# Kernel tuning notes

Measured on AMD Instinct MI355X. Metric: run time of the kernel, lower is better.

## Reference

```python
import jax, jax.numpy as jnp
import numpy as np

D_MODEL = 512
N_HEADS = 8
D_K = D_MODEL // N_HEADS  # 64
EPS = 1e-5


def setup_inputs() -> dict:
    key = jax.random.key(0)
    ks = jax.random.split(key, 16)
    s = 0.02
    B, T = 4, 2048
    return {
        "x": jax.random.normal(ks[0], (B, T, D_MODEL), dtype=jnp.float32),
        # per-head q/k/v projections stacked over heads: [H, d_model, d_k]
        "Wq": jax.random.normal(ks[1], (N_HEADS, D_MODEL, D_K), dtype=jnp.float32) * s,
        "bq": jnp.zeros((N_HEADS, D_K), dtype=jnp.float32),
        "Wk": jax.random.normal(ks[2], (N_HEADS, D_MODEL, D_K), dtype=jnp.float32) * s,
        "bk": jnp.zeros((N_HEADS, D_K), dtype=jnp.float32),
        "Wv": jax.random.normal(ks[3], (N_HEADS, D_MODEL, D_K), dtype=jnp.float32) * s,
        "bv": jnp.zeros((N_HEADS, D_K), dtype=jnp.float32),
        "Wp": jax.random.normal(ks[4], (D_MODEL, D_MODEL), dtype=jnp.float32) * s,
        "bp": jnp.zeros((D_MODEL,), dtype=jnp.float32),
        "W1": jax.random.normal(ks[5], (D_MODEL, 4 * D_MODEL), dtype=jnp.float32) * s,
        "b1": jnp.zeros((4 * D_MODEL,), dtype=jnp.float32),
        "W2": jax.random.normal(ks[6], (4 * D_MODEL, D_MODEL), dtype=jnp.float32) * s,
        "b2": jnp.zeros((D_MODEL,), dtype=jnp.float32),
        "g1": jnp.ones((D_MODEL,), dtype=jnp.float32),
        "be1": jnp.zeros((D_MODEL,), dtype=jnp.float32),
        "g2": jnp.ones((D_MODEL,), dtype=jnp.float32),
        "be2": jnp.zeros((D_MODEL,), dtype=jnp.float32),
    }


def _layer_norm(x, g, b):
    mu = jnp.mean(x, axis=-1, keepdims=True)
    var = jnp.var(x, axis=-1, keepdims=True)
    return (x - mu) * jax.lax.rsqrt(var + EPS) * g + b


def _block(x, Wq, bq, Wk, bk, Wv, bv, Wp, bp, W1, b1, W2, b2, g1, be1, g2, be2):
    B, T, _ = x.shape
    h = _layer_norm(x, g1, be1)
    # batched per-head projections: [B, H, T, d_k]
    q = jnp.einsum('btd,hdk->bhtk', h, Wq) + bq[:, None, :]
    k = jnp.einsum('btd,hdk->bhtk', h, Wk) + bk[:, None, :]
    v = jnp.einsum('btd,hdk->bhtk', h, Wv) + bv[:, None, :]
    scores = jnp.einsum('bhtk,bhsk->bhts', q, k)  # [B, H, T, T]
    causal = jnp.tril(jnp.ones((T, T), dtype=bool))
    # faithful to source: mask with -1e9 BEFORE dividing by sqrt(d_k)
    scores = jnp.where(causal, scores, jnp.float32(-1e9))
    attn = jax.nn.softmax(scores / jnp.float32(np.sqrt(D_K)), axis=-1)
    o = jnp.einsum('bhts,bhsk->bhtk', attn, v)  # [B, H, T, d_k]
    o = o.transpose(0, 2, 1, 3).reshape(B, T, D_MODEL)  # concat heads
    x = x + o @ Wp + bp
    h2 = _layer_norm(x, g2, be2)
    ff = jax.nn.relu(h2 @ W1 + b1) @ W2 + b2
    return x + ff


def reference(x, Wq, bq, Wk, bk, Wv, bv, Wp, bp, W1, b1, W2, b2, g1, be1, g2, be2):
    return _block(x, Wq, bq, Wk, bk, Wv, bv, Wp, bp, W1, b1, W2, b2, g1, be1, g2, be2)
```

## Files before the change

### kernel.cpp

```cpp
#include <hip/hip_runtime.h>
#include <hip/hip_bf16.h>
#include <math.h>

#define BATCH 4
#define SEQ   2048
#define DM    512
#define NH    8
#define DK    64
#define FF    2048
#define BT    (BATCH * SEQ)

#define SCALE_Q 0.18033688011112042f

typedef short bf16x8 __attribute__((ext_vector_type(8)));
typedef float f32x4  __attribute__((ext_vector_type(4)));

static __device__ inline short f2bf(float f) {
  union { float f; unsigned u; } v; v.f = f;
  unsigned r = (v.u + 0x7fffu + ((v.u >> 16) & 1u)) >> 16;
  return (short)r;
}

static __device__ __forceinline__ void gload16(const short* g, short* l) {
  __builtin_amdgcn_global_load_lds(
      (const __attribute__((address_space(1))) void*)g,
      (__attribute__((address_space(3))) void*)l, 16, 0, 0);
}

static __device__ __forceinline__ void xcd_swizzle(int& bx, int& by) {
  int gx = gridDim.x;
  int nwg = gx * gridDim.y;
  int id = blockIdx.x + gx * blockIdx.y;
  int nid = (id & 7) * (nwg >> 3) + (id >> 3);
  bx = nid % gx;
  by = nid / gx;
}

__global__ __launch_bounds__(256) void ln_kernel(
    const float* __restrict__ x, const float* __restrict__ gamma,
    const float* __restrict__ beta, short* __restrict__ out) {
  int row = blockIdx.x;
  const float* xr = x + (size_t)row * DM;
  int t = threadIdx.x;
  float v0 = xr[t], v1 = xr[t + 256];
  float s = v0 + v1;
  float sq = v0 * v0 + v1 * v1;
  for (int off = 32; off; off >>= 1) {
    s  += __shfl_xor(s, off);
    sq += __shfl_xor(sq, off);
  }
  __shared__ float ssum[4], ssq[4];
  int wave = t >> 6, lane = t & 63;
  if (lane == 0) { ssum[wave] = s; ssq[wave] = sq; }
  __syncthreads();
  if (t == 0) {
    float S = ssum[0] + ssum[1] + ssum[2] + ssum[3];
    float Q = ssq[0] + ssq[1] + ssq[2] + ssq[3];
    float mu = S * (1.0f / DM);
    float var = Q * (1.0f / DM) - mu * mu;
    ssum[0] = mu;
    ssq[0] = rsqrtf(var + 1e-5f);
  }
  __syncthreads();
  float mu = ssum[0], rstd = ssq[0];
  short* orow = out + (size_t)row * DM;
  orow[t]       = f2bf((v0 - mu) * rstd * gamma[t]       + beta[t]);
  orow[t + 256] = f2bf((v1 - mu) * rstd * gamma[t + 256] + beta[t + 256]);
}

__global__ __launch_bounds__(256) void wconv_kernel(
    const float* Wq, const float* Wk, const float* Wv,
    const float* Wp, const float* W1, const float* W2,
    short* wqkv, short* wpt, short* w1t, short* w2t) {
  int id = blockIdx.x;
  const float* src; short* dst; int R, C, tx, ty;
  if (id < 192) {
    int z = id >> 3;
    int m = z >> 3, hh = z & 7;
    const float* s0 = (m == 0) ? Wq : (m == 1) ? Wk : Wv;
    src = s0 + (size_t)hh * 512 * 64;
    dst = wqkv + ((size_t)(m * 512 + hh * 64)) * 512;
    R = 512; C = 64; tx = 0; ty = id & 7;
  } else if (id < 256) {
    int w = id - 192; src = Wp; dst = wpt; R = 512; C = 512;
    tx = w & 7; ty = w >> 3;
  } else if (id < 512) {
    int w = id - 256; src = W1; dst = w1t; R = 512; C = 2048;
    tx = w & 31; ty = w >> 5;
  } else {
    int w = id - 512; src = W2; dst = w2t; R = 2048; C = 512;
    tx = w & 7; ty = w >> 3;
  }
  __shared__ float Ts[64][68];
  int t = threadIdx.x;
  int r = t >> 2, c0 = (t & 3) * 16;
  const float* sp = src + (size_t)(ty * 64 + r) * C + tx * 64 + c0;
#pragma unroll
  for (int i = 0; i < 16; i += 4) {
    float4 v = *(const float4*)(sp + i);
    Ts[c0 + i + 0][r] = v.x; Ts[c0 + i + 1][r] = v.y;
    Ts[c0 + i + 2][r] = v.z; Ts[c0 + i + 3][r] = v.w;
  }
  __syncthreads();
  short* dp = dst + (size_t)(tx * 64 + r) * R + ty * 64 + c0;
  short tmp[16];
#pragma unroll
  for (int i = 0; i < 16; ++i) tmp[i] = f2bf(Ts[r][c0 + i]);
  *(int4*)(dp)     = *(int4*)&tmp[0];
  *(int4*)(dp + 8) = *(int4*)&tmp[8];
}

template<int TM, int TN>
__device__ __forceinline__ void gemm_core(
    const short* __restrict__ A, const short* __restrict__ Bw,
    int m0, int n0, int K, short* smem, f32x4 (&acc)[TM / 32][TN / 32]) {
  constexpr int AF = TM / 32, BF = TN / 32;
  constexpr int AC = TM / 64, BC = TN / 64;
  constexpr int BUFS = (TM + TN) * 32;
  int t = threadIdx.x;
  int wave = t >> 6, lane = t & 63, quad = lane >> 4, l16 = lane & 15;
  int wr = wave >> 1, wc = wave & 1;

  size_t aoff[AC], boff[BC];
  int aldsoff[AC], bldsoff[BC];
#pragma unroll
  for (int c = 0; c < AC; ++c) {
    int p = c * 256 + t, row = p >> 2, lg = (p & 3) ^ ((row >> 1) & 3);
    aoff[c] = (size_t)(m0 + row) * K + lg * 8;
    aldsoff[c] = c * 2048 + wave * 512;
  }
#pragma unroll
  for (int c = 0; c < BC; ++c) {
    int p = c * 256 + t, row = p >> 2, lg = (p & 3) ^ ((row >> 1) & 3);
    boff[c] = (size_t)(n0 + row) * K + lg * 8;
    bldsoff[c] = TM * 32 + c * 2048 + wave * 512;
  }

#pragma unroll
  for (int c = 0; c < AC; ++c) gload16(A + aoff[c], smem + aldsoff[c]);
#pragma unroll
  for (int c = 0; c < BC; ++c) gload16(Bw + boff[c], smem + bldsoff[c]);

  int physo = (quad ^ ((l16 >> 1) & 3)) * 8;

  for (int k0 = 0; k0 < K; k0 += 32) {
    short* cbuf = smem + ((k0 >> 5) & 1) * BUFS;
    __syncthreads();
    if (k0 + 32 < K) {
      short* nbuf = smem + (((k0 >> 5) & 1) ^ 1) * BUFS;
#pragma unroll
      for (int c = 0; c < AC; ++c) gload16(A + aoff[c] + k0 + 32, nbuf + aldsoff[c]);
#pragma unroll
      for (int c = 0; c < BC; ++c) gload16(Bw + boff[c] + k0 + 32, nbuf + bldsoff[c]);
    }
    bf16x8 af[AF], bfr[BF];
#pragma unroll
    for (int i = 0; i < AF; ++i)
      af[i] = *(const bf16x8*)&cbuf[(wr * (TM / 2) + i * 16 + l16) * 32 + physo];
#pragma unroll
    for (int j = 0; j < BF; ++j)
      bfr[j] = *(const bf16x8*)&cbuf[TM * 32 + (wc * (TN / 2) + j * 16 + l16) * 32 + physo];
#pragma unroll
    for (int i = 0; i < AF; ++i)
#pragma unroll
      for (int j = 0; j < BF; ++j)
        acc[i][j] = __builtin_amdgcn_mfma_f32_16x16x32_bf16(bfr[j], af[i], acc[i][j], 0, 0, 0);
  }
}

__global__ __launch_bounds__(256) void mgemm64_kernel(
    const short* __restrict__ A, const short* __restrict__ Bw,
    const float* __restrict__ bias, const float* __restrict__ res,
    void* __restrict__ C, int N, int K, int dorelu, int bf16out) {
  __shared__ __align__(16) short smem[2 * 8192];
  f32x4 acc[2][2];
  f32x4 zf = {0.f, 0.f, 0.f, 0.f};
#pragma unroll
  for (int i = 0; i < 2; ++i)
#pragma unroll
    for (int j = 0; j < 2; ++j) acc[i][j] = zf;
  int bx, by;
  xcd_swizzle(bx, by);
  int m0 = by * 64, n0 = bx * 64;

  int t = threadIdx.x;
  int wave = t >> 6, lane = t & 63, quad = lane >> 4, l16 = lane & 15;
  int wr = wave >> 1, wc = wave & 1;

  int rA0 = t >> 3,        lg0 = (t & 7) ^ (rA0 & 7);
  int rA1 = 32 + (t >> 3), lg1 = (t & 7) ^ (rA1 & 7);
  size_t aoff0 = (size_t)(m0 + rA0) * K + lg0 * 8;
  size_t aoff1 = (size_t)(m0 + rA1) * K + lg1 * 8;
  size_t boff0 = (size_t)(n0 + rA0) * K + lg0 * 8;
  size_t boff1 = (size_t)(n0 + rA1) * K + lg1 * 8;
  int lo0 = wave * 512, lo1 = 2048 + wave * 512;

  gload16(A + aoff0, smem + lo0);
  gload16(A + aoff1, smem + lo1);
  gload16(Bw + boff0, smem + 4096 + lo0);
  gload16(Bw + boff1, smem + 4096 + lo1);

  int sw = l16 & 7;

  for (int k0 = 0; k0 < K; k0 += 64) {
    short* cbuf = smem + ((k0 >> 6) & 1) * 8192;
    __syncthreads();
    if (k0 + 64 < K) {
      short* nbuf = smem + (((k0 >> 6) & 1) ^ 1) * 8192;
      gload16(A + aoff0 + k0 + 64, nbuf + lo0);
      gload16(A + aoff1 + k0 + 64, nbuf + lo1);
      gload16(Bw + boff0 + k0 + 64, nbuf + 4096 + lo0);
      gload16(Bw + boff1 + k0 + 64, nbuf + 4096 + lo1);
    }
    bf16x8 af0[2], af1[2], bf0[2], bf1[2];
#pragma unroll
    for (int i = 0; i < 2; ++i) {
      int r = wr * 32 + i * 16 + l16;
      af0[i] = *(const bf16x8*)&cbuf[r * 64 + ((quad ^ sw) * 8)];
      af1[i] = *(const bf16x8*)&cbuf[r * 64 + (((4 + quad) ^ sw) * 8)];
    }
#pragma unroll
    for (int j = 0; j < 2; ++j) {
      int r = wc * 32 + j * 16 + l16;
      bf0[j] = *(const bf16x8*)&cbuf[4096 + r * 64 + ((quad ^ sw) * 8)];
      bf1[j] = *(const bf16x8*)&cbuf[4096 + r * 64 + (((4 + quad) ^ sw) * 8)];
    }
#pragma unroll
    for (int i = 0; i < 2; ++i)
#pragma unroll
      for (int j = 0; j < 2; ++j) {
        acc[i][j] = __builtin_amdgcn_mfma_f32_16x16x32_bf16(bf0[j], af0[i], acc[i][j], 0, 0, 0);
        acc[i][j] = __builtin_amdgcn_mfma_f32_16x16x32_bf16(bf1[j], af1[i], acc[i][j], 0, 0, 0);
      }
  }

#pragma unroll
  for (int i = 0; i < 2; ++i) {
    int m = m0 + wr * 32 + i * 16 + l16;
#pragma unroll
    for (int j = 0; j < 2; ++j) {
      int nb = n0 + wc * 32 + j * 16 + quad * 4;
      float4 bv = *(const float4*)&bias[nb];
      float v[4] = {acc[i][j][0] + bv.x, acc[i][j][1] + bv.y,
                    acc[i][j][2] + bv.z, acc[i][j][3] + bv.w};
      if (dorelu) {
#pragma unroll
        for (int r = 0; r < 4; ++r) v[r] = fmaxf(v[r], 0.0f);
      }
      size_t off = (size_t)m * N + nb;
      if (res) {
        float4 rv = *(const float4*)(res + off);
        v[0] += rv.x; v[1] += rv.y; v[2] += rv.z; v[3] += rv.w;
      }
      if (bf16out) {
        short tmp[4] = {f2bf(v[0]), f2bf(v[1]), f2bf(v[2]), f2bf(v[3])};
        *(int2*)((short*)C + off) = *(int2*)tmp;
      } else {
        float4 outv = {v[0], v[1], v[2], v[3]};
        *(float4*)((float*)C + off) = outv;
      }
    }
  }
}

__global__ __launch_bounds__(256) void qkv_kernel(
    const short* __restrict__ A, const short* __restrict__ Bw,
    const float* __restrict__ bq, const float* __restrict__ bk,
    const float* __restrict__ bv,
    short* __restrict__ q, short* __restrict__ k, short* __restrict__ vt) {
  __shared__ __align__(16) short smem[12288];
  f32x4 acc[4][2];
  f32x4 zf = {0.f, 0.f, 0.f, 0.f};
#pragma unroll
  for (int i = 0; i < 4; ++i)
#pragma unroll
    for (int j = 0; j < 2; ++j) acc[i][j] = zf;
  int bx, by;
  xcd_swizzle(bx, by);
  int m0 = by * 128, n0 = bx * 64;
  gemm_core<128, 64>(A, Bw, m0, n0, DM, smem, acc);

  int t = threadIdx.x;
  int wave = t >> 6, lane = t & 63, quad = lane >> 4, l16 = lane & 15;
  int wr = wave >> 1, wc = wave & 1;

  if (n0 < 1024) {
    short* out = (n0 < 512) ? q : k;
    const float* bias = (n0 < 512) ? bq + n0 : bk + (n0 - 512);
    float scale = (n0 < 512) ? SCALE_Q : 1.0f;
    int ncol0 = (n0 < 512) ? n0 : n0 - 512;
#pragma unroll
    for (int i = 0; i < 4; ++i) {
      int m = m0 + wr * 64 + i * 16 + l16;
#pragma unroll
      for (int j = 0; j < 2; ++j) {
        int nb = wc * 32 + j * 16 + quad * 4;
        float4 bvv = *(const float4*)&bias[nb];
        short tmp[4];
        tmp[0] = f2bf((acc[i][j][0] + bvv.x) * scale);
        tmp[1] = f2bf((acc[i][j][1] + bvv.y) * scale);
        tmp[2] = f2bf((acc[i][j][2] + bvv.z) * scale);
        tmp[3] = f2bf((acc[i][j][3] + bvv.w) * scale);
        *(int2*)(out + (size_t)m * DM + ncol0 + nb) = *(int2*)tmp;
      }
    }
  } else {
    const float* bias = bv + (n0 - 1024);
    __syncthreads();
    short* Ts = smem;
#pragma unroll
    for (int i = 0; i < 4; ++i) {
      int ml = wr * 64 + i * 16 + l16;
#pragma unroll
      for (int j = 0; j < 2; ++j) {
        int nb = wc * 32 + j * 16 + quad * 4;
        float4 bvv = *(const float4*)&bias[nb];
        Ts[(nb + 0) * 136 + ml] = f2bf(acc[i][j][0] + bvv.x);
        Ts[(nb + 1) * 136 + ml] = f2bf(acc[i][j][1] + bvv.y);
        Ts[(nb + 2) * 136 + ml] = f2bf(acc[i][j][2] + bvv.z);
        Ts[(nb + 3) * 136 + ml] = f2bf(acc[i][j][3] + bvv.w);
      }
    }
    __syncthreads();
    int nl = t >> 2, seg = (t & 3) * 32;
    int gn = (n0 - 1024) + nl;
    int hh = gn >> 6, dk = gn & 63;
    int bidx = m0 >> 11, s0 = (m0 & 2047) + seg;
    short* dst = vt + ((size_t)((bidx * NH + hh) * DK + dk)) * SEQ + s0;
    const short* srcT = &Ts[nl * 136 + seg];
#pragma unroll
    for (int i2 = 0; i2 < 32; i2 += 8)
      *(int4*)(dst + i2) = *(const int4*)(srcT + i2);
  }
}

template<bool DIAG>
static __device__ __forceinline__ void attn_tile(
    const short* __restrict__ KsC, const short* __restrict__ VsC,
    short* __restrict__ Psw, const bf16x8& qf0, const bf16x8& qf1,
    f32x4 (&o_acc)[4], float& l_part, int quad, int l16,
    int keyb0, int qrow) {
  f32x4 zf = {0.f, 0.f, 0.f, 0.f};
  int sw = l16 & 7;

#pragma unroll
  for (int nt = 0; nt < 4; ++nt) {
    int krow = nt * 16 + l16;
    bf16x8 ka0 = *(const bf16x8*)&KsC[krow * 64 + ((quad ^ sw) * 8)];
    bf16x8 ka1 = *(const bf16x8*)&KsC[krow * 64 + (((4 + quad) ^ sw) * 8)];
    f32x4 s = __builtin_amdgcn_mfma_f32_16x16x32_bf16(ka0, qf0, zf, 0, 0, 0);
    s = __builtin_amdgcn_mfma_f32_16x16x32_bf16(ka1, qf1, s, 0, 0, 0);
    int keyb = keyb0 + nt * 16 + quad * 4;
    float pr[4];
#pragma unroll
    for (int r = 0; r < 4; ++r) {
      float e = exp2f(s[r]);
      pr[r] = (DIAG && (keyb + r > qrow)) ? 0.0f : e;
      l_part += pr[r];
    }
    unsigned pk0 = __builtin_amdgcn_perm(
        __float_as_uint(pr[1]), __float_as_uint(pr[0]), 0x07060302u);
    unsigned pk1 = __builtin_amdgcn_perm(
        __float_as_uint(pr[3]), __float_as_uint(pr[2]), 0x07060302u);
    int2 w = {(int)pk0, (int)pk1};
    *(int2*)&Psw[l16 * 64 + (((nt * 2 + (quad >> 1)) ^ sw) << 3) +
                 ((quad & 1) * 4)] = w;
  }

  bf16x8 apf0 = *(const bf16x8*)&Psw[l16 * 64 + ((quad ^ sw) * 8)];
  bf16x8 apf1 = *(const bf16x8*)&Psw[l16 * 64 + (((4 + quad) ^ sw) * 8)];
  __builtin_amdgcn_s_setprio(1);
#pragma unroll
  for (int nt2 = 0; nt2 < 4; ++nt2) {
    int vrow = nt2 * 16 + l16;
    bf16x8 vf0 = *(const bf16x8*)&VsC[vrow * 64 + ((quad ^ sw) * 8)];
    bf16x8 vf1 = *(const bf16x8*)&VsC[vrow * 64 + (((4 + quad) ^ sw) * 8)];
    o_acc[nt2] = __builtin_amdgcn_mfma_f32_16x16x32_bf16(vf0, apf0, o_acc[nt2], 0, 0, 0);
    o_acc[nt2] = __builtin_amdgcn_mfma_f32_16x16x32_bf16(vf1, apf1, o_acc[nt2], 0, 0, 0);
  }
  __builtin_amdgcn_s_setprio(0);
}

__global__ __launch_bounds__(256) void fattn_kernel(
    const short* __restrict__ Q, const short* __restrict__ Kg,
    const short* __restrict__ Vt, short* __restrict__ O) {
  int id = blockIdx.x + 32 * (blockIdx.y + NH * blockIdx.z);
  int c = id & 7, j = id >> 3;
  int g = c * 4 + (j & 3);
  int qt = 31 - (j >> 2);
  int h = g & 7, b = g >> 3;
  int q0 = qt * 64;
  int t = threadIdx.x, wave = t >> 6, lane = t & 63, quad = lane >> 4, l16 = lane & 15;

  __shared__ __align__(16) short Ks[2][64 * 64];
  __shared__ __align__(16) short Vs[2][64 * 64];
  __shared__ __align__(16) short Ps[4][16 * 64];

  f32x4 zf = {0.f, 0.f, 0.f, 0.f};
  const short* qp = Q + ((size_t)(b * SEQ + q0 + wave * 16 + l16)) * DM + h * DK;
  bf16x8 qf0 = *(const bf16x8*)(qp + quad * 8);
  bf16x8 qf1 = *(const bf16x8*)(qp + 32 + quad * 8);

  f32x4 o_acc[4];
  float l_part = 0.0f;
#pragma unroll
  for (int i = 0; i < 4; ++i) o_acc[i] = zf;

  const short* kb = Kg + ((size_t)(b * SEQ)) * DM + h * DK;
  const short* vb = Vt + ((size_t)((b * NH + h) * DK)) * SEQ;

  int row0 = t >> 3,         lg0 = (t & 7) ^ (row0 & 7);
  int row1 = (256 + t) >> 3, lg1 = ((256 + t) & 7) ^ (row1 & 7);
  const short* kp0 = kb + (size_t)row0 * DM + lg0 * 8;
  const short* kp1 = kb + (size_t)row1 * DM + lg1 * 8;
  const short* vp0 = vb + (size_t)row0 * SEQ + lg0 * 8;
  const short* vp1 = vb + (size_t)row1 * SEQ + lg1 * 8;
  int lo0 = wave * 512, lo1 = 2048 + wave * 512;

#define STAGE_KV(B) do {                                     \
    gload16(kp0, &Ks[B][lo0]); gload16(kp1, &Ks[B][lo1]);    \
    gload16(vp0, &Vs[B][lo0]); gload16(vp1, &Vs[B][lo1]);    \
    kp0 += 64 * DM; kp1 += 64 * DM; vp0 += 64; vp1 += 64; } while (0)

  STAGE_KV(0);

  int qrow = q0 + wave * 16 + l16;
  short* Psw = &Ps[wave][0];

  int buf = 0;
  for (int kt = 0; kt < qt; ++kt) {
    __syncthreads();
    STAGE_KV(buf ^ 1);
    attn_tile<false>(&Ks[buf][0], &Vs[buf][0], Psw, qf0, qf1,
                     o_acc, l_part, quad, l16, 0, qrow);
    buf ^= 1;
  }
  __syncthreads();
  attn_tile<true>(&Ks[buf][0], &Vs[buf][0], Psw, qf0, qf1,
                  o_acc, l_part, quad, l16, qt * 64, qrow);

  float lf = l_part;
  lf += __shfl_xor(lf, 16);
  lf += __shfl_xor(lf, 32);
  float inv = 1.0f / lf;
  short* orow = O + ((size_t)(b * SEQ) + qrow) * DM + h * DK;
#pragma unroll
  for (int nt2 = 0; nt2 < 4; ++nt2) {
    short tmp[4];
#pragma unroll
    for (int r = 0; r < 4; ++r) tmp[r] = f2bf(o_acc[nt2][r] * inv);
    *(int2*)(orow + nt2 * 16 + quad * 4) = *(int2*)tmp;
  }
#undef STAGE_KV
}

extern "C" void kernel_launch(void* const* d_in, const int* in_sizes, int n_in,
                              void* d_out, int out_size, void* d_ws, size_t ws_size,
                              hipStream_t stream) {
  const float* x   = (const float*)d_in[0];
  const float* Wq  = (const float*)d_in[1];
  const float* bq  = (const float*)d_in[2];
  const float* Wk  = (const float*)d_in[3];
  const float* bk  = (const float*)d_in[4];
  const float* Wv  = (const float*)d_in[5];
  const float* bv  = (const float*)d_in[6];
  const float* Wp  = (const float*)d_in[7];
  const float* bp  = (const float*)d_in[8];
  const float* W1  = (const float*)d_in[9];
  const float* b1  = (const float*)d_in[10];
  const float* W2  = (const float*)d_in[11];
  const float* b2  = (const float*)d_in[12];
  const float* g1  = (const float*)d_in[13];
  const float* be1 = (const float*)d_in[14];
  const float* g2  = (const float*)d_in[15];
  const float* be2 = (const float*)d_in[16];
  float* out = (float*)d_out;

  char* wsb = (char*)d_ws;
  const size_t SB = (size_t)BT * DM * 2;
  short* h    = (short*)(wsb);
  short* q    = (short*)(wsb + SB);
  short* k    = (short*)(wsb + 2 * SB);
  short* vt   = (short*)(wsb + 3 * SB);
  short* o    = (short*)(wsb + 4 * SB);
  float* x2   = (float*)(wsb + 5 * SB);
  short* h2   = (short*)(wsb + 5 * SB + (size_t)BT * DM * 4);
  short* ff   = (short*)(wsb + 6 * SB + (size_t)BT * DM * 4);
  short* wqkv = (short*)(wsb + 6 * SB + (size_t)BT * DM * 4 + (size_t)BT * FF * 2);
  short* wpt  = wqkv + 1536 * 512;
  short* w1t  = wpt + 512 * 512;
  short* w2t  = w1t + 2048 * 512;

  dim3 blk(256);

  wconv_kernel<<<dim3(768), blk, 0, stream>>>(Wq, Wk, Wv, Wp, W1, W2,
                                              wqkv, wpt, w1t, w2t);
  ln_kernel<<<BT, blk, 0, stream>>>(x, g1, be1, h);

  qkv_kernel<<<dim3(24, 64), blk, 0, stream>>>(h, wqkv, bq, bk, bv, q, k, vt);

  fattn_kernel<<<dim3(32, NH, BATCH), blk, 0, stream>>>(q, k, vt, o);

  mgemm64_kernel<<<dim3(8, 128), blk, 0, stream>>>(o, wpt, bp, x, x2, DM, DM, 0, 0);
  ln_kernel<<<BT, blk, 0, stream>>>(x2, g2, be2, h2);
  mgemm64_kernel<<<dim3(32, 128), blk, 0, stream>>>(h2, w1t, b1, nullptr, ff, FF, DM, 1, 1);
  mgemm64_kernel<<<dim3(8, 128), blk, 0, stream>>>(ff, w2t, b2, x2, out, DM, FF, 0, 0);
}
```

Baseline: 254.5 us.

## Split long causal attention query tiles across two blocks with a combine pass

Query tiles 16-31 are split into two key ranges (tiles 0-15 and 16-diagonal) handled by separate blocks. Each half writes unnormalized fp32 partial outputs and row sums to scratch that reuses the FF buffer, and a new combine kernel sums them and normalizes. The aim is to even out per-block work in causal attention and raise the block count from 1024 to 1536, cutting the tail where a few long blocks run alone. The cost is an extra kernel launch and extra fp32 scratch traffic. Adding the two partials directly is only valid because the kernel uses no per-row running max rescaling.

```diff
diff --git a/kernel.cpp b/kernel.cpp
--- a/kernel.cpp
+++ b/kernel.cpp
@@ -383,12 +383,19 @@
 
 __global__ __launch_bounds__(256) void fattn_kernel(
     const short* __restrict__ Q, const short* __restrict__ Kg,
-    const short* __restrict__ Vt, short* __restrict__ O) {
-  int id = blockIdx.x + 32 * (blockIdx.y + NH * blockIdx.z);
+    const short* __restrict__ Vt, short* __restrict__ O,
+    float* __restrict__ pscr) {
+  int id = blockIdx.x;
   int c = id & 7, j = id >> 3;
-  int g = c * 4 + (j & 3);
-  int qt = 31 - (j >> 2);
+  int sub = j & 3, w = j >> 2;
+  int g = c * 4 + sub;
   int h = g & 7, b = g >> 3;
+  int qt, kt0, ktN, p = 0;
+  bool split;
+  if (w < 16)      { qt = 31 - w;        p = 0; kt0 = 0;  ktN = 16;     split = true;  }
+  else if (w < 32) { qt = 31 - (w - 16); p = 1; kt0 = 16; ktN = qt + 1; split = true;  }
+  else             { qt = 15 - (w - 32);        kt0 = 0;  ktN = qt + 1; split = false; }
+  bool hasdiag = !(split && p == 0);
   int q0 = qt * 64;
   int t = threadIdx.x, wave = t >> 6, lane = t & 63, quad = lane >> 4, l16 = lane & 15;
 
@@ -411,10 +418,10 @@
 
   int row0 = t >> 3,         lg0 = (t & 7) ^ (row0 & 7);
   int row1 = (256 + t) >> 3, lg1 = ((256 + t) & 7) ^ (row1 & 7);
-  const short* kp0 = kb + (size_t)row0 * DM + lg0 * 8;
-  const short* kp1 = kb + (size_t)row1 * DM + lg1 * 8;
-  const short* vp0 = vb + (size_t)row0 * SEQ + lg0 * 8;
-  const short* vp1 = vb + (size_t)row1 * SEQ + lg1 * 8;
+  const short* kp0 = kb + (size_t)row0 * DM + lg0 * 8 + (size_t)kt0 * 64 * DM;
+  const short* kp1 = kb + (size_t)row1 * DM + lg1 * 8 + (size_t)kt0 * 64 * DM;
+  const short* vp0 = vb + (size_t)row0 * SEQ + lg0 * 8 + kt0 * 64;
+  const short* vp1 = vb + (size_t)row1 * SEQ + lg1 * 8 + kt0 * 64;
   int lo0 = wave * 512, lo1 = 2048 + wave * 512;
 
 #define STAGE_KV(B) do {                                     \
@@ -428,7 +435,7 @@
   short* Psw = &Ps[wave][0];
 
   int buf = 0;
-  for (int kt = 0; kt < qt; ++kt) {
+  for (int kt = kt0; kt < ktN - 1; ++kt) {
     __syncthreads();
     STAGE_KV(buf ^ 1);
     attn_tile<false>(&Ks[buf][0], &Vs[buf][0], Psw, qf0, qf1,
@@ -436,22 +443,55 @@
     buf ^= 1;
   }
   __syncthreads();
-  attn_tile<true>(&Ks[buf][0], &Vs[buf][0], Psw, qf0, qf1,
-                  o_acc, l_part, quad, l16, qt * 64, qrow);
+  if (hasdiag)
+    attn_tile<true>(&Ks[buf][0], &Vs[buf][0], Psw, qf0, qf1,
+                    o_acc, l_part, quad, l16, (ktN - 1) * 64, qrow);
+  else
+    attn_tile<false>(&Ks[buf][0], &Vs[buf][0], Psw, qf0, qf1,
+                     o_acc, l_part, quad, l16, 0, qrow);
 
   float lf = l_part;
   lf += __shfl_xor(lf, 16);
   lf += __shfl_xor(lf, 32);
-  float inv = 1.0f / lf;
-  short* orow = O + ((size_t)(b * SEQ) + qrow) * DM + h * DK;
-#pragma unroll
-  for (int nt2 = 0; nt2 < 4; ++nt2) {
-    short tmp[4];
-#pragma unroll
-    for (int r = 0; r < 4; ++r) tmp[r] = f2bf(o_acc[nt2][r] * inv);
-    *(int2*)(orow + nt2 * 16 + quad * 4) = *(int2*)tmp;
+
+  if (!split) {
+    float inv = 1.0f / lf;
+    short* orow = O + ((size_t)(b * SEQ) + qrow) * DM + h * DK;
+#pragma unroll
+    for (int nt2 = 0; nt2 < 4; ++nt2) {
+      short tmp[4];
+#pragma unroll
+      for (int r = 0; r < 4; ++r) tmp[r] = f2bf(o_acc[nt2][r] * inv);
+      *(int2*)(orow + nt2 * 16 + quad * 4) = *(int2*)tmp;
+    }
+  } else {
+    int pblk = g * 16 + (qt - 16);
+    int srow = pblk * 64 + wave * 16 + l16;
+    float* po = pscr + (size_t)p * (32768 * 64);
+    float* pl = pscr + (size_t)2 * (32768 * 64) + (size_t)p * 32768;
+#pragma unroll
+    for (int nt2 = 0; nt2 < 4; ++nt2)
+      *(f32x4*)&po[(size_t)srow * 64 + nt2 * 16 + quad * 4] = o_acc[nt2];
+    if (lane < 16) pl[pblk * 64 + wave * 16 + lane] = lf;
   }
 #undef STAGE_KV
+}
+
+__global__ __launch_bounds__(256) void cmb_kernel(
+    const float* __restrict__ pscr, short* __restrict__ O) {
+  int gid = blockIdx.x * 256 + threadIdx.x;
+  int srow = gid >> 6, dk = gid & 63;
+  const float* po0 = pscr;
+  const float* po1 = pscr + (size_t)32768 * 64;
+  const float* pl0 = pscr + (size_t)2 * 32768 * 64;
+  const float* pl1 = pl0 + 32768;
+  float v = po0[gid] + po1[gid];
+  float l = pl0[srow] + pl1[srow];
+  int g = srow >> 10, rem = srow & 1023;
+  int qt = 16 + (rem >> 6), row = rem & 63;
+  int b = g >> 3, h = g & 7;
+  int qrow = qt * 64 + row;
+  O[((size_t)(b * SEQ + qrow)) * DM + h * DK + dk] = f2bf(v / l);
 }
 
 extern "C" void kernel_launch(void* const* d_in, const int* in_sizes, int n_in,
@@ -486,6 +526,7 @@
   float* x2   = (float*)(wsb + 5 * SB);
   short* h2   = (short*)(wsb + 5 * SB + (size_t)BT * DM * 4);
   short* ff   = (short*)(wsb + 6 * SB + (size_t)BT * DM * 4);
+  float* pscr = (float*)ff;
   short* wqkv = (short*)(wsb + 6 * SB + (size_t)BT * DM * 4 + (size_t)BT * FF * 2);
   short* wpt  = wqkv + 1536 * 512;
   short* w1t  = wpt + 512 * 512;
@@ -499,7 +540,8 @@
 
   qkv_kernel<<<dim3(24, 64), blk, 0, stream>>>(h, wqkv, bq, bk, bv, q, k, vt);
 
-  fattn_kernel<<<dim3(32, NH, BATCH), blk, 0, stream>>>(q, k, vt, o);
+  fattn_kernel<<<dim3(1536), blk, 0, stream>>>(q, k, vt, o, pscr);
+  cmb_kernel<<<dim3(8192), blk, 0, stream>>>(pscr, o);
 
   mgemm64_kernel<<<dim3(8, 128), blk, 0, stream>>>(o, wpt, bp, x, x2, DM, DM, 0, 0);
   ln_kernel<<<BT, blk, 0, stream>>>(x2, g2, be2, h2);
```

After: 251.4 us. No clear change (-1.2%).
